# Kernel optimization log

Measured on AMD Instinct MI355X. Metric: run time of the kernel, lower is better.

## Reference

```python
import jax, jax.numpy as jnp
import numpy as np

# Model config (mirrors init_kwargs)
N_HEADS = 32
N_KV_HEADS = 8
HEAD_DIM = 128
DIM = 4096
FREQ_BASE = 500000.0
MAX_SEQ_LEN = 8192
B = 16
T = 16


def _ggml_rope(x, pos):
    """ggml-style RoPE (mode 0): rotates adjacent pairs (x[2i], x[2i+1]).
    x: [B, T, H, HEAD_DIM], pos: [T] int."""
    half = HEAD_DIM // 2
    inv_freq = FREQ_BASE ** (-(jnp.arange(half, dtype=jnp.float32) * 2.0) / HEAD_DIM)  # [half]
    ang = pos.astype(jnp.float32)[:, None] * inv_freq[None, :]                        # [T, half]
    cos = jnp.cos(ang)[None, :, None, :]  # [1, T, 1, half]
    sin = jnp.sin(ang)[None, :, None, :]
    xr = x.reshape(*x.shape[:-1], half, 2)
    x0, x1 = xr[..., 0], xr[..., 1]
    o0 = x0 * cos - x1 * sin
    o1 = x0 * sin + x1 * cos
    return jnp.stack([o0, o1], axis=-1).reshape(x.shape)


def setup_inputs() -> dict:
    key = jax.random.key(0)
    ks = jax.random.split(key, 10)
    x = jax.random.normal(ks[0], (B, T, DIM), dtype=jnp.float32)
    # decode step at the end of the cache -> kv_len == MAX_SEQ_LEN (static)
    input_pos = jnp.arange(MAX_SEQ_LEN - T, MAX_SEQ_LEN, dtype=jnp.int32)
    # causal mask over the full cache: query i may attend to positions <= input_pos[i]
    js = jnp.arange(MAX_SEQ_LEN)
    attn_mask = jnp.where(js[None, :] <= input_pos[:, None], 0.0, -jnp.inf).astype(jnp.float32)  # [T, kv_len]
    k_cache = jax.random.normal(ks[1], (B, MAX_SEQ_LEN, N_KV_HEADS, HEAD_DIM), dtype=jnp.float32)
    v_cache = jax.random.normal(ks[2], (B, MAX_SEQ_LEN, N_KV_HEADS, HEAD_DIM), dtype=jnp.float32)
    s = 1.0 / np.sqrt(DIM)
    wq = jax.random.normal(ks[3], (N_HEADS * HEAD_DIM, DIM), dtype=jnp.float32) * s
    wk = jax.random.normal(ks[4], (N_KV_HEADS * HEAD_DIM, DIM), dtype=jnp.float32) * s
    wv = jax.random.normal(ks[5], (N_KV_HEADS * HEAD_DIM, DIM), dtype=jnp.float32) * s
    wo = jax.random.normal(ks[6], (DIM, N_HEADS * HEAD_DIM), dtype=jnp.float32) * s
    # freqs_cos/freqs_sin are in the torch forward signature but unused (ggml.rope
    # recomputes them from input_pos + freq_base); kept as dummy inputs.
    half = HEAD_DIM // 2
    freqs_cos = jax.random.uniform(ks[7], (T, half), dtype=jnp.float32)
    freqs_sin = jax.random.uniform(ks[8], (T, half), dtype=jnp.float32)
    return {"x": x, "freqs_cos": freqs_cos, "freqs_sin": freqs_sin,
            "input_pos": input_pos, "attn_mask": attn_mask,
            "k_cache": k_cache, "v_cache": v_cache,
            "wq": wq, "wk": wk, "wv": wv, "wo": wo}


def reference(x, freqs_cos, freqs_sin, input_pos, attn_mask, k_cache, v_cache, wq, wk, wv, wo):
    Bx, Tx, _ = x.shape
    n_rep = N_HEADS // N_KV_HEADS
    q = jnp.einsum('btd,ed->bte', x, wq).reshape(Bx, Tx, N_HEADS, HEAD_DIM)
    k = jnp.einsum('btd,ed->bte', x, wk).reshape(Bx, Tx, N_KV_HEADS, HEAD_DIM)
    v = jnp.einsum('btd,ed->bte', x, wv).reshape(Bx, Tx, N_KV_HEADS, HEAD_DIM)
    q = _ggml_rope(q, input_pos)
    k = _ggml_rope(k, input_pos)
    # KV-cache index_copy along time axis
    k_cache = k_cache.at[:, input_pos].set(k)
    v_cache = v_cache.at[:, input_pos].set(v)
    # kv_len = input_pos[0] + T == MAX_SEQ_LEN here (static), so use full cache.
    kq = k_cache  # [B, S, Hkv, D]
    vq = v_cache
    scale = 1.0 / np.sqrt(HEAD_DIM)
    # GQA: group q heads as [g=n_kv, r=n_rep]; equivalent to repeat_interleave on K/V
    qg = q.reshape(Bx, Tx, N_KV_HEADS, n_rep, HEAD_DIM)
    scores = jnp.einsum('btgrd,bsgd->bgrts', qg, kq) * scale  # [B, g, r, T, S]
    scores = scores + attn_mask  # [T, S] broadcasts
    attn = jax.nn.softmax(scores, axis=-1)
    y = jnp.einsum('bgrts,bsgd->btgrd', attn, vq).reshape(Bx, Tx, N_HEADS * HEAD_DIM)
    return jnp.einsum('bte,de->btd', y, wo)
```

## Files before the change

kernel.cpp:

```cpp
#include <hip/hip_runtime.h>
#include <math.h>

#define SEQ 8192
#define NEWBASE 8176
#define NS 4

typedef short s16x4 __attribute__((ext_vector_type(4)));
typedef short s16x8 __attribute__((ext_vector_type(8)));
typedef float f32x4 __attribute__((ext_vector_type(4)));

__device__ __forceinline__ short f2bf(float f) {
  unsigned u = __float_as_uint(f);
  u += 0x7FFFu + ((u >> 16) & 1u);
  return (short)(u >> 16);
}

__device__ __forceinline__ f32x4 mfma16(s16x8 a, s16x8 b, f32x4 c) {
  return __builtin_amdgcn_mfma_f32_16x16x32_bf16(a, b, c, 0, 0, 0);
}

__device__ __forceinline__ void sync_nodrain() {
  __builtin_amdgcn_sched_barrier(0);
  asm volatile("s_waitcnt lgkmcnt(0)" ::: "memory");
  __builtin_amdgcn_s_barrier();
  __builtin_amdgcn_sched_barrier(0);
}

template<int KS>
__device__ __forceinline__
void gemm_tile_pc(const float* __restrict__ A, const float* __restrict__ Bw,
                  float* __restrict__ Cp, int ldc) {
  __shared__ short As[2][64 * 72];
  __shared__ short Bs[2][128 * 72];
  const int tid = threadIdx.x, lane = tid & 63, w = tid >> 6;
  const int l15 = lane & 15, l4 = lane >> 4;

  if (w < 4) {
    float4 aA[4], aB[4], bA[8], bB[8];
    auto issue = [&](int st, float4 (&ar)[4], float4 (&br)[8]) {
      const float* Ab = A + st * 64;
      const float* Bb = Bw + st * 64;
#pragma unroll
      for (int i = 0; i < 4; ++i) {
        int id = tid + i * 256;
        ar[i] = *(const float4*)(Ab + (size_t)(id >> 4) * 4096 + ((id & 15) << 2));
      }
#pragma unroll
      for (int i = 0; i < 8; ++i) {
        int id = tid + i * 256;
        br[i] = *(const float4*)(Bb + (size_t)(id >> 4) * 4096 + ((id & 15) << 2));
      }
    };
    auto convert = [&](int buf, const float4 (&ar)[4], const float4 (&br)[8]) {
#pragma unroll
      for (int i = 0; i < 4; ++i) {
        int id = tid + i * 256, row = id >> 4, c4 = (id & 15) << 2;
        s16x4 h = { f2bf(ar[i].x), f2bf(ar[i].y), f2bf(ar[i].z), f2bf(ar[i].w) };
        *(s16x4*)&As[buf][row * 72 + c4] = h;
      }
#pragma unroll
      for (int i = 0; i < 8; ++i) {
        int id = tid + i * 256, row = id >> 4, c4 = (id & 15) << 2;
        s16x4 h = { f2bf(br[i].x), f2bf(br[i].y), f2bf(br[i].z), f2bf(br[i].w) };
        *(s16x4*)&Bs[buf][row * 72 + c4] = h;
      }
    };

    issue(0, aA, bA);
    issue(1, aB, bB);
    convert(0, aA, bA);
    sync_nodrain();
    for (int c = 1; c < KS; c += 2) {
      convert(1, aB, bB);
      if (c + 1 < KS) issue(c + 1, aA, bA);
      sync_nodrain();
      if (c + 1 < KS) convert(0, aA, bA);
      if (c + 2 < KS) issue(c + 2, aB, bB);
      sync_nodrain();
    }
  } else {
    const int cw = w - 4;
    f32x4 acc[8] = {};
    sync_nodrain();
    for (int c = 0; c < KS; ++c) {
      const short* Ab = &As[c & 1][0];
      const short* Bb = &Bs[c & 1][0];
#pragma unroll
      for (int kk = 0; kk < 64; kk += 32) {
        s16x8 a = *(const s16x8*)&Ab[(cw * 16 + l15) * 72 + kk + l4 * 8];
#pragma unroll
        for (int nf = 0; nf < 8; ++nf) {
          s16x8 b = *(const s16x8*)&Bb[(nf * 16 + l15) * 72 + kk + l4 * 8];
          acc[nf] = mfma16(a, b, acc[nf]);
        }
      }
      sync_nodrain();
    }
#pragma unroll
    for (int nf = 0; nf < 8; ++nf)
#pragma unroll
      for (int r = 0; r < 4; ++r)
        Cp[(size_t)(cw * 16 + l4 * 4 + r) * ldc + nf * 16 + l15] = acc[nf][r];
  }
}

__global__ __launch_bounds__(512)
__attribute__((amdgpu_waves_per_eu(4, 4)))
void gemm_qkv(const float* __restrict__ x,
              const float* __restrict__ wq, const float* __restrict__ wk,
              const float* __restrict__ wv, float* __restrict__ part,
              const int* __restrict__ ipos,
              float* __restrict__ ctab, float* __restrict__ stab) {
  int bn = blockIdx.x, bm = blockIdx.y, sp = blockIdx.z;
  if (bn == 0 && bm == 0 && sp == 0) {
#pragma unroll
    for (int k = 0; k < 2; ++k) {
      int i = threadIdx.x + k * 512;
      int t = i >> 6, f = i & 63;
      double inv = exp(-((double)(2 * f) / 128.0) * log(500000.0));
      double ang = (double)ipos[t] * inv;
      ctab[i] = (float)cos(ang);
      stab[i] = (float)sin(ang);
    }
  }
  const float* Bw;
  if (bn < 32)      Bw = wq + (size_t)(bn * 128) * 4096;
  else if (bn < 40) Bw = wk + (size_t)((bn - 32) * 128) * 4096;
  else              Bw = wv + (size_t)((bn - 40) * 128) * 4096;
  const float* A = x + (size_t)(bm * 64) * 4096 + sp * 1024;
  float* Cp = part + (size_t)sp * (256 * 6144) + (size_t)(bm * 64) * 6144 + bn * 128;
  gemm_tile_pc<16>(A, Bw + sp * 1024, Cp, 6144);
}

__global__ __launch_bounds__(512)
__attribute__((amdgpu_waves_per_eu(4, 4)))
void gemm_out(const float* __restrict__ y, const float* __restrict__ wo,
              float* __restrict__ part) {
  int bn = blockIdx.x, bm = blockIdx.y, sp = blockIdx.z;
  const float* A = y + (size_t)(bm * 64) * 4096 + sp * 1024;
  const float* Bw = wo + (size_t)(bn * 128) * 4096 + sp * 1024;
  float* Cp = part + (size_t)sp * (256 * 4096) + (size_t)(bm * 64) * 4096 + bn * 128;
  gemm_tile_pc<16>(A, Bw, Cp, 4096);
}

__global__ __launch_bounds__(256)
void rope_reduce(const float* __restrict__ part, const float* __restrict__ ctab,
                 const float* __restrict__ stab, float* __restrict__ q,
                 float* __restrict__ kn, float* __restrict__ vn) {
  int idx = blockIdx.x * 256 + threadIdx.x;
  int m = idx / 3072;
  int col = (idx - m * 3072) * 2;
  const float* src = part + (size_t)m * 6144 + col;
  float a0 = 0.f, a1 = 0.f;
#pragma unroll
  for (int s = 0; s < 4; ++s) {
    a0 += src[(size_t)s * 1572864];
    a1 += src[(size_t)s * 1572864 + 1];
  }
  if (col < 5120) {
    int local = (col < 4096) ? col : col - 4096;
    int f = (local & 127) >> 1, t = m & 15;
    float c = ctab[t * 64 + f], sn = stab[t * 64 + f];
    float o0 = a0 * c - a1 * sn, o1 = a0 * sn + a1 * c;
    if (col < 4096) {
      q[(size_t)m * 4096 + col] = o0;
      q[(size_t)m * 4096 + col + 1] = o1;
    } else {
      kn[(size_t)m * 1024 + local] = o0;
      kn[(size_t)m * 1024 + local + 1] = o1;
    }
  } else {
    int local = col - 5120;
    vn[(size_t)m * 1024 + local] = a0;
    vn[(size_t)m * 1024 + local + 1] = a1;
  }
}

__global__ __launch_bounds__(512)
__attribute__((amdgpu_waves_per_eu(4, 4)))
void attn7(const float* __restrict__ kc_, const float* __restrict__ vc_,
           const float* __restrict__ qb, const float* __restrict__ kn,
           const float* __restrict__ vn, const int* __restrict__ ipos,
           float* __restrict__ pO, float* __restrict__ pL) {
  __shared__ short Ks[2][32 * 128];
  __shared__ short Vt[2][128 * 34];
  __shared__ short Ps[4 * 16 * 40];
  const int sh = blockIdx.x, g = blockIdx.y, b = blockIdx.z;
  const int tid = threadIdx.x, lane = tid & 63, w = tid >> 6;
  const int l15 = lane & 15, l4 = lane >> 4;
  const float scale = 0.08838834764831845f;
  const int sbase = sh * 2048;

  const float* kc_b = kc_ + (size_t)b * SEQ * 1024 + g * 128;
  const float* vc_b = vc_ + (size_t)b * SEQ * 1024 + g * 128;
  const float* kn_b = kn + (size_t)b * 16 * 1024 + g * 128;
  const float* vn_b = vn + (size_t)b * 16 * 1024 + g * 128;

  if (w < 4) {
    const int krow = tid >> 5, kc4 = (tid & 31) << 2;
    const int vcol = tid & 127, vhr = (tid >> 7) << 4;
    float4 kA[4], kB[4];
    float vA[16], vB[16];

    auto issue = [&](int cb, float4 (&kr)[4], float (&vr)[16]) {
      if (cb + 32 <= NEWBASE) {
#pragma unroll
        for (int i = 0; i < 4; ++i)
          kr[i] = *(const float4*)(kc_b + (size_t)(cb + krow + i * 8) * 1024 + kc4);
#pragma unroll
        for (int j = 0; j < 16; ++j)
          vr[j] = vc_b[(size_t)(cb + vhr + j) * 1024 + vcol];
      } else {
#pragma unroll
        for (int i = 0; i < 4; ++i) {
          int sg = cb + krow + i * 8;
          const float* src = (sg >= NEWBASE)
              ? (kn_b + (size_t)(sg - NEWBASE) * 1024 + kc4)
              : (kc_b + (size_t)sg * 1024 + kc4);
          kr[i] = *(const float4*)src;
        }
#pragma unroll
        for (int j = 0; j < 16; ++j) {
          int sg = cb + vhr + j;
          vr[j] = (sg >= NEWBASE)
              ? vn_b[(size_t)(sg - NEWBASE) * 1024 + vcol]
              : vc_b[(size_t)sg * 1024 + vcol];
        }
      }
    };
    auto convert = [&](int buf, const float4 (&kr)[4], const float (&vr)[16]) {
#pragma unroll
      for (int i = 0; i < 4; ++i) {
        int s = krow + i * 8;
        s16x4 hv = { f2bf(kr[i].x), f2bf(kr[i].y), f2bf(kr[i].z), f2bf(kr[i].w) };
        *(s16x4*)&Ks[buf][s * 128 + (kc4 ^ ((s & 7) << 3))] = hv;
      }
#pragma unroll
      for (int j4 = 0; j4 < 4; ++j4) {
        s16x4 hv = { f2bf(vr[j4 * 4]), f2bf(vr[j4 * 4 + 1]),
                     f2bf(vr[j4 * 4 + 2]), f2bf(vr[j4 * 4 + 3]) };
        *(s16x4*)&Vt[buf][vcol * 34 + vhr + j4 * 4] = hv;
      }
    };

    issue(sbase, kA, vA);
    issue(sbase + 32, kB, vB);
    convert(0, kA, vA);
    sync_nodrain();
    for (int c = 1; c < 64; c += 2) {
      convert(1, kB, vB);
      if (c + 1 < 64) issue(sbase + (c + 1) * 32, kA, vA);
      sync_nodrain();
      if (c + 1 < 64) convert(0, kA, vA);
      if (c + 2 < 64) issue(sbase + (c + 2) * 32, kB, vB);
      sync_nodrain();
    }
  } else {
    const int qg = w - 4;
    s16x8 qa[4];
    {
      int qr = qg * 16 + l15;
      int t = qr >> 2, r = qr & 3, h = g * 4 + r;
      const float* qp = qb + (size_t)(b * 16 + t) * 4096 + h * 128;
#pragma unroll
      for (int ks = 0; ks < 4; ++ks) {
        float4 v0 = *(const float4*)(qp + ks * 32 + l4 * 8);
        float4 v1 = *(const float4*)(qp + ks * 32 + l4 * 8 + 4);
        qa[ks] = s16x8{ f2bf(v0.x), f2bf(v0.y), f2bf(v0.z), f2bf(v0.w),
                        f2bf(v1.x), f2bf(v1.y), f2bf(v1.z), f2bf(v1.w) };
      }
    }
    const int ip_t = ipos[qg * 4 + l4];
    f32x4 o[8] = {};
    float lsum[4] = { 0.f, 0.f, 0.f, 0.f };
    short* Pw = &Ps[qg * (16 * 40)];

    sync_nodrain();
    for (int c = 0; c < 64; ++c) {
      const short* Kb = &Ks[c & 1][0];
      const short* Vb = &Vt[c & 1][0];
      const int base = sbase + c * 32;
      f32x4 sc[2] = {};
#pragma unroll
      for (int ks = 0; ks < 4; ++ks) {
        int dd = ks * 32 + l4 * 8;
#pragma unroll
        for (int nf = 0; nf < 2; ++nf) {
          int s = nf * 16 + l15;
          s16x8 kb = *(const s16x8*)&Kb[s * 128 + (dd ^ ((s & 7) << 3))];
          sc[nf] = mfma16(qa[ks], kb, sc[nf]);
        }
      }
#pragma unroll
      for (int nf = 0; nf < 2; ++nf) {
        int sg = base + nf * 16 + l15;
#pragma unroll
        for (int r = 0; r < 4; ++r) {
          float p = (sg <= ip_t) ? __expf(sc[nf][r] * scale) : 0.f;
          lsum[r] += p;
          Pw[(l4 * 4 + r) * 40 + nf * 16 + l15] = f2bf(p);
        }
      }
      s16x8 pa = *(const s16x8*)&Pw[l15 * 40 + l4 * 8];
#pragma unroll
      for (int nd = 0; nd < 8; ++nd) {
        int d = nd * 16 + l15;
        s16x8 vb = *(const s16x8*)&Vb[d * 34 + l4 * 8];
        o[nd] = mfma16(pa, vb, o[nd]);
      }
      sync_nodrain();
    }
#pragma unroll
    for (int r = 0; r < 4; ++r) {
      lsum[r] += __shfl_xor(lsum[r], 1, 64);
      lsum[r] += __shfl_xor(lsum[r], 2, 64);
      lsum[r] += __shfl_xor(lsum[r], 4, 64);
      lsum[r] += __shfl_xor(lsum[r], 8, 64);
    }
    const int blk = (b * 8 + g) * NS + sh;
    float* Ob = pO + (size_t)blk * 64 * 128;
#pragma unroll
    for (int nd = 0; nd < 8; ++nd)
#pragma unroll
      for (int r = 0; r < 4; ++r)
        Ob[(qg * 16 + l4 * 4 + r) * 128 + nd * 16 + l15] = o[nd][r];
    if (l15 == 0) {
#pragma unroll
      for (int r = 0; r < 4; ++r)
        pL[blk * 64 + qg * 16 + l4 * 4 + r] = lsum[r];
    }
  }
}

__global__ __launch_bounds__(256)
void merge(const float* __restrict__ pO, const float* __restrict__ pL,
           float* __restrict__ y) {
  const int gq = blockIdx.x, b = blockIdx.y;
  const int g = gq >> 2, qc = gq & 3;
  const int bb = (b * 8 + g) * NS;
#pragma unroll
  for (int i = 0; i < 8; ++i) {
    int id = qc * 2048 + i * 256 + threadIdx.x;
    int qr = id >> 7, d = id & 127;
    float acc = 0.f, den = 0.f;
#pragma unroll
    for (int p = 0; p < NS; ++p) {
      acc += pO[(size_t)(bb + p) * 8192 + id];
      den += pL[(bb + p) * 64 + qr];
    }
    int t = qr >> 2, r = qr & 3, h = g * 4 + r;
    y[(size_t)(b * 16 + t) * 4096 + h * 128 + d] = acc / den;
  }
}

__global__ __launch_bounds__(256)
void out_reduce(const float* __restrict__ part, float* __restrict__ out) {
  int i = blockIdx.x * 256 + threadIdx.x;
  const f32x4* p4 = (const f32x4*)part;
  f32x4 s = {0.f, 0.f, 0.f, 0.f};
#pragma unroll
  for (int sp = 0; sp < 4; ++sp) s += p4[(size_t)sp * 262144 + i];
  ((f32x4*)out)[i] = s;
}

extern "C" void kernel_launch(void* const* d_in, const int* in_sizes, int n_in,
                              void* d_out, int out_size, void* d_ws, size_t ws_size,
                              hipStream_t stream) {
  const float* x      = (const float*)d_in[0];
  const int*   ipos   = (const int*)d_in[3];
  const float* kcache = (const float*)d_in[5];
  const float* vcache = (const float*)d_in[6];
  const float* wq     = (const float*)d_in[7];
  const float* wk     = (const float*)d_in[8];
  const float* wv     = (const float*)d_in[9];
  const float* wo     = (const float*)d_in[10];
  float* out = (float*)d_out;

  float* q_buf = (float*)d_ws;
  float* k_new = q_buf + 1048576;
  float* v_new = k_new + 262144;
  float* y_buf = v_new + 262144;
  float* ctab  = y_buf + 1048576;
  float* stab  = ctab + 1024;
  float* pO    = stab + 1024;
  float* pL    = pO + 8388608;
  float* qkvp  = pO;
  float* outp  = pO;

  gemm_qkv<<<dim3(48, 4, 4), 512, 0, stream>>>(x, wq, wk, wv, qkvp,
                                               ipos, ctab, stab);
  rope_reduce<<<3072, 256, 0, stream>>>(qkvp, ctab, stab, q_buf, k_new, v_new);
  attn7<<<dim3(NS, 8, 16), 512, 0, stream>>>(kcache, vcache, q_buf, k_new, v_new,
                                             ipos, pO, pL);
  merge<<<dim3(32, 16), 256, 0, stream>>>(pO, pL, y_buf);
  gemm_out<<<dim3(32, 4, 4), 512, 0, stream>>>(y_buf, wo, outp);
  out_reduce<<<1024, 256, 0, stream>>>(outp, out);
}
```

Baseline: 293.3 us.

## Fuse split-KV merge into output projection GEMM A-tile loading

After: 334.9 us. 1.14x slower.

```diff
diff --git a/kernel.cpp b/kernel.cpp
--- a/kernel.cpp
+++ b/kernel.cpp
@@ -134,13 +134,92 @@
 
 __global__ __launch_bounds__(512)
 __attribute__((amdgpu_waves_per_eu(4, 4)))
-void gemm_out(const float* __restrict__ y, const float* __restrict__ wo,
-              float* __restrict__ part) {
-  int bn = blockIdx.x, bm = blockIdx.y, sp = blockIdx.z;
-  const float* A = y + (size_t)(bm * 64) * 4096 + sp * 1024;
+void gemm_out_fused(const float* __restrict__ pO, const float* __restrict__ pL,
+                    const float* __restrict__ wo, float* __restrict__ part) {
+  __shared__ short As[2][64 * 72];
+  __shared__ short Bs[2][128 * 72];
+  const int bn = blockIdx.x, bm = blockIdx.y, sp = blockIdx.z;
+  const int tid = threadIdx.x, lane = tid & 63, w = tid >> 6;
+  const int l15 = lane & 15, l4 = lane >> 4;
   const float* Bw = wo + (size_t)(bn * 128) * 4096 + sp * 1024;
   float* Cp = part + (size_t)sp * (256 * 4096) + (size_t)(bm * 64) * 4096 + bn * 128;
-  gemm_tile_pc<16>(A, Bw, Cp, 4096);
+
+  if (w < 4) {
+    float4 bA[8], bB[8];
+    auto issueB = [&](int st, float4 (&br)[8]) {
+      const float* Bb = Bw + st * 64;
+#pragma unroll
+      for (int i = 0; i < 8; ++i) {
+        int id = tid + i * 256;
+        br[i] = *(const float4*)(Bb + (size_t)(id >> 4) * 4096 + ((id & 15) << 2));
+      }
+    };
+    auto convert = [&](int buf, int st, const float4 (&br)[8]) {
+#pragma unroll
+      for (int i = 0; i < 4; ++i) {
+        int id = tid + i * 256, rl = id >> 4, c4 = (id & 15) << 2;
+        int gcol = sp * 1024 + st * 64 + c4;
+        int row = bm * 64 + rl, bb = row >> 4, t = row & 15;
+        int h = gcol >> 7, g = h >> 2, rep = h & 3;
+        int qr = t * 4 + rep;
+        int blk = (bb * 8 + g) * NS;
+        const float* pp = pO + (size_t)blk * 8192 + qr * 128 + (gcol & 127);
+        f32x4 s0 = *(const f32x4*)pp;
+        f32x4 s1 = *(const f32x4*)(pp + 8192);
+        f32x4 s2 = *(const f32x4*)(pp + 16384);
+        f32x4 s3 = *(const f32x4*)(pp + 24576);
+        const float* lp = pL + blk * 64 + qr;
+        float den = lp[0] + lp[64] + lp[128] + lp[192];
+        f32x4 s = (s0 + s1) + (s2 + s3);
+        float rd = 1.0f / den;
+        s16x4 hh = { f2bf(s[0] * rd), f2bf(s[1] * rd),
+                     f2bf(s[2] * rd), f2bf(s[3] * rd) };
+        *(s16x4*)&As[buf][rl * 72 + c4] = hh;
+      }
+#pragma unroll
+      for (int i = 0; i < 8; ++i) {
+        int id = tid + i * 256, rowb = id >> 4, c4 = (id & 15) << 2;
+        s16x4 h = { f2bf(br[i].x), f2bf(br[i].y), f2bf(br[i].z), f2bf(br[i].w) };
+        *(s16x4*)&Bs[buf][rowb * 72 + c4] = h;
+      }
+    };
+
+    issueB(0, bA);
+    issueB(1, bB);
+    convert(0, 0, bA);
+    sync_nodrain();
+    for (int c = 1; c < 16; c += 2) {
+      convert(1, c, bB);
+      if (c + 1 < 16) issueB(c + 1, bA);
+      sync_nodrain();
+      if (c + 1 < 16) convert(0, c + 1, bA);
+      if (c + 2 < 16) issueB(c + 2, bB);
+      sync_nodrain();
+    }
+  } else {
+    const int cw = w - 4;
+    f32x4 acc[8] = {};
+    sync_nodrain();
+    for (int c = 0; c < 16; ++c) {
+      const short* Ab = &As[c & 1][0];
+      const short* Bb = &Bs[c & 1][0];
+#pragma unroll
+      for (int kk = 0; kk < 64; kk += 32) {
+        s16x8 a = *(const s16x8*)&Ab[(cw * 16 + l15) * 72 + kk + l4 * 8];
+#pragma unroll
+        for (int nf = 0; nf < 8; ++nf) {
+          s16x8 b = *(const s16x8*)&Bb[(nf * 16 + l15) * 72 + kk + l4 * 8];
+          acc[nf] = mfma16(a, b, acc[nf]);
+        }
+      }
+      sync_nodrain();
+    }
+#pragma unroll
+    for (int nf = 0; nf < 8; ++nf)
+#pragma unroll
+      for (int r = 0; r < 4; ++r)
+        Cp[(size_t)(cw * 16 + l4 * 4 + r) * 4096 + nf * 16 + l15] = acc[nf][r];
+  }
 }
 
 __global__ __launch_bounds__(256)
@@ -333,27 +412,6 @@
 }
 
 __global__ __launch_bounds__(256)
-void merge(const float* __restrict__ pO, const float* __restrict__ pL,
-           float* __restrict__ y) {
-  const int gq = blockIdx.x, b = blockIdx.y;
-  const int g = gq >> 2, qc = gq & 3;
-  const int bb = (b * 8 + g) * NS;
-#pragma unroll
-  for (int i = 0; i < 8; ++i) {
-    int id = qc * 2048 + i * 256 + threadIdx.x;
-    int qr = id >> 7, d = id & 127;
-    float acc = 0.f, den = 0.f;
-#pragma unroll
-    for (int p = 0; p < NS; ++p) {
-      acc += pO[(size_t)(bb + p) * 8192 + id];
-      den += pL[(bb + p) * 64 + qr];
-    }
-    int t = qr >> 2, r = qr & 3, h = g * 4 + r;
-    y[(size_t)(b * 16 + t) * 4096 + h * 128 + d] = acc / den;
-  }
-}
-
-__global__ __launch_bounds__(256)
 void out_reduce(const float* __restrict__ part, float* __restrict__ out) {
   int i = blockIdx.x * 256 + threadIdx.x;
   const f32x4* p4 = (const f32x4*)part;
@@ -385,14 +443,13 @@
   float* pO    = stab + 1024;
   float* pL    = pO + 8388608;
   float* qkvp  = pO;
-  float* outp  = pO;
+  float* outp  = pO + 4194304;
 
   gemm_qkv<<<dim3(48, 4, 4), 512, 0, stream>>>(x, wq, wk, wv, qkvp,
                                                ipos, ctab, stab);
   rope_reduce<<<3072, 256, 0, stream>>>(qkvp, ctab, stab, q_buf, k_new, v_new);
   attn7<<<dim3(NS, 8, 16), 512, 0, stream>>>(kcache, vcache, q_buf, k_new, v_new,
                                              ipos, pO, pL);
-  merge<<<dim3(32, 16), 256, 0, stream>>>(pO, pL, y_buf);
-  gemm_out<<<dim3(32, 4, 4), 512, 0, stream>>>(y_buf, wo, outp);
+  gemm_out_fused<<<dim3(32, 4, 4), 512, 0, stream>>>(pO, pL, wo, outp);
   out_reduce<<<1024, 256, 0, stream>>>(outp, out);
 }
```
